# Performance work log

Hardware: AMD Instinct MI355X
Metric: run time of the kernel (lower is better)

## Reference

```python
import jax, jax.numpy as jnp
import numpy as np

IN_DIM, HID, OUT_DIM, NUM_LAYERS = 768, 512, 768, 4
B, T = 128, 256
EPS = 1e-5


def setup_inputs() -> dict:
    key = jax.random.key(0)
    ks = jax.random.split(key, 16)
    s = 0.02
    inp = {
        "x": jax.random.normal(ks[0], (B, T, IN_DIM), dtype=jnp.float32),
        "h0": jnp.zeros((NUM_LAYERS, B, HID), dtype=jnp.float32),
        "c0": jnp.zeros((NUM_LAYERS, B, HID), dtype=jnp.float32),
        "W_in": jax.random.normal(ks[1], (HID, IN_DIM), dtype=jnp.float32) * s,
        "b_in": jnp.zeros((HID,), dtype=jnp.float32),
        # stacked LSTM weights: all layers take HID input (after input_proj)
        "W_ih": jax.random.normal(ks[2], (NUM_LAYERS, 4 * HID, HID), dtype=jnp.float32) * s,
        "W_hh": jax.random.normal(ks[3], (NUM_LAYERS, 4 * HID, HID), dtype=jnp.float32) * s,
        "b_ih": jnp.zeros((NUM_LAYERS, 4 * HID), dtype=jnp.float32),
        "b_hh": jnp.zeros((NUM_LAYERS, 4 * HID), dtype=jnp.float32),
        "W_out": jax.random.normal(ks[4], (OUT_DIM, HID), dtype=jnp.float32) * s,
        "b_out": jnp.zeros((OUT_DIM,), dtype=jnp.float32),
        "ln_g": jnp.ones((OUT_DIM,), dtype=jnp.float32),
        "ln_b": jnp.zeros((OUT_DIM,), dtype=jnp.float32),
    }
    return inp


def _lstm_layer(x_seq, h0, c0, Wih, Whh, bih, bhh):
    # x_seq: [B,T,H] -> outputs [B,T,H], (hT, cT)
    bias = bih + bhh  # fuse the two biases

    def step(carry, x_t):
        h, c = carry
        gates = x_t @ Wih.T + h @ Whh.T + bias  # [B,4H]
        i, f, g, o = jnp.split(gates, 4, axis=-1)  # PyTorch gate order i,f,g,o
        i = jax.nn.sigmoid(i)
        f = jax.nn.sigmoid(f)
        g = jnp.tanh(g)
        o = jax.nn.sigmoid(o)
        c = f * c + i * g
        h = o * jnp.tanh(c)
        return (h, c), h

    (hT, cT), hs = jax.lax.scan(step, (h0, c0), jnp.swapaxes(x_seq, 0, 1))
    return jnp.swapaxes(hs, 0, 1), hT, cT


def reference(x, h0, c0, W_in, b_in, W_ih, W_hh, b_ih, b_hh, W_out, b_out, ln_g, ln_b):
    # input projection
    h = x @ W_in.T + b_in  # [B,T,HID]
    h_finals, c_finals = [], []
    for l in range(NUM_LAYERS):  # fixed small layer count; dropout inactive (eval)
        h, hT, cT = _lstm_layer(h, h0[l], c0[l], W_ih[l], W_hh[l], b_ih[l], b_hh[l])
        h_finals.append(hT)
        c_finals.append(cT)
    out = h @ W_out.T + b_out  # [B,T,OUT]
    mu = jnp.mean(out, axis=-1, keepdims=True)
    var = jnp.mean(jnp.square(out - mu), axis=-1, keepdims=True)
    out = (out - mu) * jax.lax.rsqrt(var + EPS) * ln_g + ln_b
    return out, jnp.stack(h_finals), jnp.stack(c_finals)
```

## Files before the change

### kernel.cpp

```cpp
#include <hip/hip_runtime.h>
#include <math.h>

#define T_SEQ 256
#define BATCH 128
#define HID 512
#define NL 4
#define HT_OFF 25165824u
#define CT_OFF 25427968u
#define HALL_ELEMS 67371008u
#define XP_ELEMS   16777216u
#define FLG_OFF(l,t) ((((l) << 8) + (t)) << 6)

typedef __attribute__((ext_vector_type(8))) short bf16x8;
typedef __attribute__((ext_vector_type(4))) float f32x4;

__device__ __forceinline__ short f2bf(float f) {
    unsigned u = __float_as_uint(f);
    u = (u + 0x7fffu + ((u >> 16) & 1u)) >> 16;
    return (short)u;
}
__device__ __forceinline__ unsigned pack2(float a, float b) {
    return ((unsigned)(unsigned short)f2bf(a)) |
           (((unsigned)(unsigned short)f2bf(b)) << 16);
}
__device__ __forceinline__ bf16x8 ld8_sc1g(const short* p) {
    unsigned long long q0 = __hip_atomic_load((const unsigned long long*)p,
                                              __ATOMIC_RELAXED, __HIP_MEMORY_SCOPE_AGENT);
    unsigned long long q1 = __hip_atomic_load((const unsigned long long*)(p + 512),
                                              __ATOMIC_RELAXED, __HIP_MEMORY_SCOPE_AGENT);
    union { unsigned long long q[2]; bf16x8 v; } u;
    u.q[0] = q0; u.q[1] = q1;
    return u.v;
}
__device__ __forceinline__ void poll_cnt4(const unsigned* base, int lane) {
    const unsigned* p = base + ((lane & 3) << 4);
    unsigned v = __hip_atomic_load(p, __ATOMIC_RELAXED, __HIP_MEMORY_SCOPE_AGENT);
    while (__any(v < 16u)) {
        __builtin_amdgcn_s_sleep(1);
        v = __hip_atomic_load(p, __ATOMIC_RELAXED, __HIP_MEMORY_SCOPE_AGENT);
    }
    asm volatile("" ::: "memory");
}
__device__ __forceinline__ void lds_wait(int* p, int want) {
    while (__hip_atomic_load(p, __ATOMIC_ACQUIRE, __HIP_MEMORY_SCOPE_WORKGROUP) < want)
        __builtin_amdgcn_s_sleep(1);
    asm volatile("" ::: "memory");
}

__global__ void init_kernel(short* __restrict__ h_all, unsigned* __restrict__ flg,
                            const float* __restrict__ h0) {
    int idx = blockIdx.x * 256 + threadIdx.x;
    if (idx < NL * BATCH * HID) {
        int l = idx >> 16, rest = idx & 65535;
        int r = rest >> 9, k = rest & 511;
        h_all[((size_t)(l * 257) << 16) + (((size_t)(k >> 2)) << 9) + (r << 2) + (k & 3)]
            = f2bf(h0[idx]);
    }
    if (idx < NL * T_SEQ * 64) flg[idx] = 0u;
}

__global__ __launch_bounds__(256) void gemm_xp(const float* __restrict__ x,
                                               const float* __restrict__ W_in,
                                               const float* __restrict__ b_in,
                                               short* __restrict__ xp) {
    __shared__ short As[128 * 72];
    __shared__ short Bs[128 * 72];
    const int tid = threadIdx.x;
    const int w = tid >> 6, lane = tid & 63;
    const int m = lane & 15, quad = lane >> 4;
    const int rowbase = blockIdx.x * 128;
    const int colbase = blockIdx.y * 128;
    f32x4 acc[2][8];
#pragma unroll
    for (int rt = 0; rt < 2; ++rt)
#pragma unroll
        for (int ct = 0; ct < 8; ++ct) { f32x4 z = {0.f,0.f,0.f,0.f}; acc[rt][ct] = z; }

    for (int k0 = 0; k0 < 768; k0 += 64) {
        __syncthreads();
#pragma unroll
        for (int i = 0; i < 8; ++i) {
            int q = tid + (i << 8);
            int r = q >> 4, f4 = (q & 15) << 2;
            float4 v = *(const float4*)(x + (size_t)(rowbase + r) * 768 + k0 + f4);
            uint2 p; p.x = pack2(v.x, v.y); p.y = pack2(v.z, v.w);
            *(uint2*)&As[r * 72 + f4] = p;
        }
#pragma unroll
        for (int i = 0; i < 8; ++i) {
            int q = tid + (i << 8);
            int r = q >> 4, f4 = (q & 15) << 2;
            float4 v = *(const float4*)(W_in + (size_t)(colbase + r) * 768 + k0 + f4);
            uint2 p; p.x = pack2(v.x, v.y); p.y = pack2(v.z, v.w);
            *(uint2*)&Bs[r * 72 + f4] = p;
        }
        __syncthreads();
#pragma unroll
        for (int ks = 0; ks < 2; ++ks) {
            int kof = (ks << 5) + (quad << 3);
            bf16x8 a0 = *(const bf16x8*)&As[((w * 2 + 0) * 16 + m) * 72 + kof];
            bf16x8 a1 = *(const bf16x8*)&As[((w * 2 + 1) * 16 + m) * 72 + kof];
#pragma unroll
            for (int ct = 0; ct < 8; ++ct) {
                bf16x8 b = *(const bf16x8*)&Bs[(ct * 16 + m) * 72 + kof];
                acc[0][ct] = __builtin_amdgcn_mfma_f32_16x16x32_bf16(a0, b, acc[0][ct], 0, 0, 0);
                acc[1][ct] = __builtin_amdgcn_mfma_f32_16x16x32_bf16(a1, b, acc[1][ct], 0, 0, 0);
            }
        }
    }
    float bias_r[8];
#pragma unroll
    for (int ct = 0; ct < 8; ++ct) bias_r[ct] = b_in[colbase + ct * 16 + m];
#pragma unroll
    for (int rt = 0; rt < 2; ++rt)
#pragma unroll
        for (int reg = 0; reg < 4; ++reg) {
            int m_glob = rowbase + (w * 2 + rt) * 16 + quad * 4 + reg;
            int t = m_glob & 255, b = m_glob >> 8;
            short* dst = xp + (((size_t)(t << 7) + b) << 9);
#pragma unroll
            for (int ct = 0; ct < 8; ++ct)
                dst[colbase + ct * 16 + m] = f2bf(acc[rt][ct][reg] + bias_r[ct]);
        }
}

__global__ __launch_bounds__(256) void gemm_out(const short* __restrict__ h3,
                                                const float* __restrict__ W_out,
                                                const float* __restrict__ b_out,
                                                float* __restrict__ out) {
    __shared__ short As[128 * 72];
    __shared__ short Bs[128 * 72];
    const int tid = threadIdx.x;
    const int w = tid >> 6, lane = tid & 63;
    const int m = lane & 15, quad = lane >> 4;
    const int rowbase = blockIdx.x * 128;
    const int colbase = blockIdx.y * 128;
    f32x4 acc[2][8];
#pragma unroll
    for (int rt = 0; rt < 2; ++rt)
#pragma unroll
        for (int ct = 0; ct < 8; ++ct) { f32x4 z = {0.f,0.f,0.f,0.f}; acc[rt][ct] = z; }

    for (int k0 = 0; k0 < 512; k0 += 64) {
        __syncthreads();
#pragma unroll
        for (int i = 0; i < 4; ++i) {
            int q = tid + (i << 8);
            int r = q >> 3, seg = (q & 7) << 3;
            *(bf16x8*)&As[r * 72 + seg] =
                *(const bf16x8*)(h3 + (size_t)(rowbase + r) * 512 + k0 + seg);
        }
#pragma unroll
        for (int i = 0; i < 8; ++i) {
            int q = tid + (i << 8);
            int r = q >> 4, f4 = (q & 15) << 2;
            float4 v = *(const float4*)(W_out + (size_t)(colbase + r) * 512 + k0 + f4);
            uint2 p; p.x = pack2(v.x, v.y); p.y = pack2(v.z, v.w);
            *(uint2*)&Bs[r * 72 + f4] = p;
        }
        __syncthreads();
#pragma unroll
        for (int ks = 0; ks < 2; ++ks) {
            int kof = (ks << 5) + (quad << 3);
            bf16x8 a0 = *(const bf16x8*)&As[((w * 2 + 0) * 16 + m) * 72 + kof];
            bf16x8 a1 = *(const bf16x8*)&As[((w * 2 + 1) * 16 + m) * 72 + kof];
#pragma unroll
            for (int ct = 0; ct < 8; ++ct) {
                bf16x8 b = *(const bf16x8*)&Bs[(ct * 16 + m) * 72 + kof];
                acc[0][ct] = __builtin_amdgcn_mfma_f32_16x16x32_bf16(a0, b, acc[0][ct], 0, 0, 0);
                acc[1][ct] = __builtin_amdgcn_mfma_f32_16x16x32_bf16(a1, b, acc[1][ct], 0, 0, 0);
            }
        }
    }
    float bias_r[8];
#pragma unroll
    for (int ct = 0; ct < 8; ++ct) bias_r[ct] = b_out[colbase + ct * 16 + m];
#pragma unroll
    for (int rt = 0; rt < 2; ++rt)
#pragma unroll
        for (int reg = 0; reg < 4; ++reg) {
            int m_glob = rowbase + (w * 2 + rt) * 16 + quad * 4 + reg;
            int t = m_glob >> 7, b = m_glob & 127;
            float* dst = out + (size_t)b * 196608 + (size_t)t * 768;
#pragma unroll
            for (int ct = 0; ct < 8; ++ct)
                dst[colbase + ct * 16 + m] = acc[rt][ct][reg] + bias_r[ct];
        }
}

__global__ __launch_bounds__(512, 2) void lstm_pipeline(
    short* __restrict__ xp, short* __restrict__ h_all,
    unsigned* __restrict__ flg,
    const float* __restrict__ W_ih, const float* __restrict__ W_hh,
    const float* __restrict__ b_ih, const float* __restrict__ b_hh,
    const float* __restrict__ c0, float* __restrict__ d_out) {
    __shared__ float gatesX[128 * 33];
    __shared__ float gatesH[128 * 33];
    __shared__ float cL[128 * 8];
    __shared__ float biasL[32];
    __shared__ int ldsdep[2];

    const int tid = threadIdx.x;
    const int l = blockIdx.x >> 6, c = blockIdx.x & 63;
    const int w = tid >> 6, lane = tid & 63;
    const int m = lane & 15, quad = lane >> 4;
    const bool hw = (w >= 4);
    const int w2 = w & 3;

    const float* Wsrc = hw ? W_hh : W_ih;
    bf16x8 wf[32];
#pragma unroll
    for (int ks = 0; ks < 16; ++ks) {
#pragma unroll
        for (int ct = 0; ct < 2; ++ct) {
            int u = ct * 16 + m;
            int gr = ((u >> 3) << 9) + (c << 3) + (u & 7);
            const float* s = Wsrc + ((size_t)(l * 2048 + gr) << 9) + ks * 32 + quad * 8;
            float4 v0 = *(const float4*)s;
            float4 v1 = *(const float4*)(s + 4);
            uint4 p;
            p.x = pack2(v0.x, v0.y); p.y = pack2(v0.z, v0.w);
            p.z = pack2(v1.x, v1.y); p.w = pack2(v1.z, v1.w);
            wf[ks * 2 + ct] = *(bf16x8*)&p;
        }
    }
    if (tid < 32) {
        int gr = ((tid >> 3) << 9) + (c << 3) + (tid & 7);
        biasL[tid] = b_ih[l * 2048 + gr] + b_hh[l * 2048 + gr];
    }
    if (tid < 2) ldsdep[tid] = 0;
    for (int p = tid; p < 1024; p += 512) {
        int r = p >> 3, hc = p & 7;
        cL[p] = c0[((size_t)l << 16) + (r << 9) + (c << 3) + hc];
    }
    __syncthreads();

    const int er = tid >> 2, eq = (tid & 3) << 1;

    for (int t = 0; t < T_SEQ; ++t) {
        if (hw) {
            if (t > 0) {
                if (w == 4) {
                    poll_cnt4(flg + FLG_OFF(l, t - 1), lane);
                    __hip_atomic_store(&ldsdep[1], t, __ATOMIC_RELEASE,
                                       __HIP_MEMORY_SCOPE_WORKGROUP);
                } else {
                    lds_wait(&ldsdep[1], t);
                }
            }
        } else if (l > 0) {
            if (w == 0) {
                poll_cnt4(flg + FLG_OFF(l - 1, t), lane);
                __hip_atomic_store(&ldsdep[0], t + 1, __ATOMIC_RELEASE,
                                   __HIP_MEMORY_SCOPE_WORKGROUP);
            } else {
                lds_wait(&ldsdep[0], t + 1);
            }
        }
        asm volatile("" ::: "memory");

        f32x4 z = {0.f, 0.f, 0.f, 0.f};
        f32x4 acc00 = z, acc01 = z, acc10 = z, acc11 = z;

        if (!hw && l == 0) {
            const short* src = xp + ((size_t)t << 16);
#pragma unroll
            for (int ks = 0; ks < 16; ++ks) {
                int ka = ks * 32 + quad * 8;
                bf16x8 a0 = *(const bf16x8*)(src + ((size_t)(w2 * 32 + m) << 9) + ka);
                bf16x8 a1 = *(const bf16x8*)(src + ((size_t)(w2 * 32 + 16 + m) << 9) + ka);
                acc00 = __builtin_amdgcn_mfma_f32_16x16x32_bf16(a0, wf[ks * 2 + 0], acc00, 0, 0, 0);
                acc01 = __builtin_amdgcn_mfma_f32_16x16x32_bf16(a0, wf[ks * 2 + 1], acc01, 0, 0, 0);
                acc10 = __builtin_amdgcn_mfma_f32_16x16x32_bf16(a1, wf[ks * 2 + 0], acc10, 0, 0, 0);
                acc11 = __builtin_amdgcn_mfma_f32_16x16x32_bf16(a1, wf[ks * 2 + 1], acc11, 0, 0, 0);
            }
        } else {
            const short* src = hw
                ? (h_all + ((size_t)(l * 257 + t) << 16))
                : (h_all + ((size_t)((l - 1) * 257 + t + 1) << 16));
#pragma unroll
            for (int ks = 0; ks < 16; ++ks) {
                int g = ks * 8 + quad * 2;
                const short* p = src + ((size_t)g << 9) + ((w2 * 32 + m) << 2);
                bf16x8 a0 = ld8_sc1g(p);
                bf16x8 a1 = ld8_sc1g(p + 64);
                acc00 = __builtin_amdgcn_mfma_f32_16x16x32_bf16(a0, wf[ks * 2 + 0], acc00, 0, 0, 0);
                acc01 = __builtin_amdgcn_mfma_f32_16x16x32_bf16(a0, wf[ks * 2 + 1], acc01, 0, 0, 0);
                acc10 = __builtin_amdgcn_mfma_f32_16x16x32_bf16(a1, wf[ks * 2 + 0], acc10, 0, 0, 0);
                acc11 = __builtin_amdgcn_mfma_f32_16x16x32_bf16(a1, wf[ks * 2 + 1], acc11, 0, 0, 0);
            }
        }
        const int gb0 = w2 * 32 + quad * 4;
        float* gdst = hw ? gatesH : gatesX;
#pragma unroll
        for (int reg = 0; reg < 4; ++reg) {
            gdst[(gb0 + reg) * 33 + m]           = acc00[reg];
            gdst[(gb0 + reg) * 33 + 16 + m]      = acc01[reg];
            gdst[(gb0 + 16 + reg) * 33 + m]      = acc10[reg];
            gdst[(gb0 + 16 + reg) * 33 + 16 + m] = acc11[reg];
        }
        __syncthreads();

        float hv[2], cv[2];
#pragma unroll
        for (int e = 0; e < 2; ++e) {
            int hc = eq + e;
            float iv = gatesX[er * 33 + hc]      + gatesH[er * 33 + hc]      + biasL[hc];
            float fv = gatesX[er * 33 + 8 + hc]  + gatesH[er * 33 + 8 + hc]  + biasL[8 + hc];
            float gv = gatesX[er * 33 + 16 + hc] + gatesH[er * 33 + 16 + hc] + biasL[16 + hc];
            float ov = gatesX[er * 33 + 24 + hc] + gatesH[er * 33 + 24 + hc] + biasL[24 + hc];
            float ig = 1.f / (1.f + __expf(-iv));
            float fg = 1.f / (1.f + __expf(-fv));
            float gg = tanhf(gv);
            float og = 1.f / (1.f + __expf(-ov));
            float cn = fg * cL[er * 8 + hc] + ig * gg;
            float hn = og * tanhf(cn);
            cL[er * 8 + hc] = cn;
            hv[e] = hn; cv[e] = cn;
        }
        unsigned pk = pack2(hv[0], hv[1]);
        {
            int g = c * 2 + (eq >> 2);
            unsigned* hdst = (unsigned*)(h_all + ((size_t)(l * 257 + t + 1) << 16)
                                         + ((size_t)g << 9) + (er << 2) + (eq & 3));
            __hip_atomic_store(hdst, pk, __ATOMIC_RELAXED, __HIP_MEMORY_SCOPE_AGENT);
        }
        if (l == 3) {
            unsigned* xdst = (unsigned*)(xp + ((size_t)t << 16) + (er << 9) + (c << 3) + eq);
            __hip_atomic_store(xdst, pk, __ATOMIC_RELAXED, __HIP_MEMORY_SCOPE_AGENT);
        }
        if (t == T_SEQ - 1) {
            size_t fo = ((size_t)l << 16) + (size_t)(er << 9) + (c << 3) + eq;
            d_out[HT_OFF + fo]     = hv[0];
            d_out[HT_OFF + fo + 1] = hv[1];
            d_out[CT_OFF + fo]     = cv[0];
            d_out[CT_OFF + fo + 1] = cv[1];
        }
        __syncthreads();
        if (tid == 0)
            __hip_atomic_fetch_add(flg + FLG_OFF(l, t) + ((c >> 4) << 4), 1u,
                                   __ATOMIC_RELAXED, __HIP_MEMORY_SCOPE_AGENT);
    }
}

__global__ __launch_bounds__(256) void ln_kernel(float* __restrict__ out,
                                                 const float* __restrict__ g,
                                                 const float* __restrict__ bvec) {
    float* p = out + (size_t)blockIdx.x * 768;
    int tid = threadIdx.x;
    float v0 = p[tid], v1 = p[tid + 256], v2 = p[tid + 512];
    float s = v0 + v1 + v2;
    float q = v0 * v0 + v1 * v1 + v2 * v2;
    for (int off = 32; off > 0; off >>= 1) {
        s += __shfl_down(s, off);
        q += __shfl_down(q, off);
    }
    __shared__ float ss[4], qq[4];
    __shared__ float mu_s, rs_s;
    int w = tid >> 6;
    if ((tid & 63) == 0) { ss[w] = s; qq[w] = q; }
    __syncthreads();
    if (tid == 0) {
        float S = ss[0] + ss[1] + ss[2] + ss[3];
        float Q = qq[0] + qq[1] + qq[2] + qq[3];
        float mu = S * (1.f / 768.f);
        float var = Q * (1.f / 768.f) - mu * mu;
        mu_s = mu;
        rs_s = rsqrtf(var + 1e-5f);
    }
    __syncthreads();
    float mu = mu_s, rs = rs_s;
    p[tid]       = (v0 - mu) * rs * g[tid]       + bvec[tid];
    p[tid + 256] = (v1 - mu) * rs * g[tid + 256] + bvec[tid + 256];
    p[tid + 512] = (v2 - mu) * rs * g[tid + 512] + bvec[tid + 512];
}

extern "C" void kernel_launch(void* const* d_in, const int* in_sizes, int n_in,
                              void* d_out, int out_size, void* d_ws, size_t ws_size,
                              hipStream_t stream) {
    (void)in_sizes; (void)n_in; (void)out_size; (void)ws_size;
    const float* x     = (const float*)d_in[0];
    const float* h0    = (const float*)d_in[1];
    const float* c0    = (const float*)d_in[2];
    const float* W_in  = (const float*)d_in[3];
    const float* b_in  = (const float*)d_in[4];
    const float* W_ih  = (const float*)d_in[5];
    const float* W_hh  = (const float*)d_in[6];
    const float* b_ih  = (const float*)d_in[7];
    const float* b_hh  = (const float*)d_in[8];
    const float* W_out = (const float*)d_in[9];
    const float* b_out = (const float*)d_in[10];
    const float* ln_g  = (const float*)d_in[11];
    const float* ln_b  = (const float*)d_in[12];

    float* out   = (float*)d_out;
    short* h_all = (short*)d_ws;
    short* xp    = h_all + HALL_ELEMS;
    unsigned* flg = (unsigned*)(xp + XP_ELEMS);

    init_kernel<<<1024, 256, 0, stream>>>(h_all, flg, h0);
    gemm_xp<<<dim3(256, 4), 256, 0, stream>>>(x, W_in, b_in, xp);
    lstm_pipeline<<<256, 512, 0, stream>>>(xp, h_all, flg, W_ih, W_hh,
                                           b_ih, b_hh, c0, out);
    gemm_out<<<dim3(256, 6), 256, 0, stream>>>(xp, W_out, b_out, out);
    ln_kernel<<<32768, 256, 0, stream>>>(out, ln_g, ln_b);
}
```

Before: 3.030 ms.

## Software-pipeline h loads, pad LDS strides, use fast tanh, relax launch bounds

Splits the recurrent matvec's global h loads into four chunks that are double-buffered, so loads of later chunks are issued while MFMAs run on earlier ones. LDS gate and cell buffers get padded strides (35 and 9) to reduce bank conflicts. tanhf is replaced by an exp-based fast tanh, which adds a small approximation error. Launch bounds drop from two blocks per CU to one, giving the compiler more registers for the extra prefetch buffers.

```diff
diff --git a/kernel.cpp b/kernel.cpp
--- a/kernel.cpp
+++ b/kernel.cpp
@@ -14,6 +14,8 @@
 typedef __attribute__((ext_vector_type(8))) short bf16x8;
 typedef __attribute__((ext_vector_type(4))) float f32x4;
 
+#define GSTR 35
+
 __device__ __forceinline__ short f2bf(float f) {
     unsigned u = __float_as_uint(f);
     u = (u + 0x7fffu + ((u >> 16) & 1u)) >> 16;
@@ -45,6 +47,10 @@
     while (__hip_atomic_load(p, __ATOMIC_ACQUIRE, __HIP_MEMORY_SCOPE_WORKGROUP) < want)
         __builtin_amdgcn_s_sleep(1);
     asm volatile("" ::: "memory");
+}
+__device__ __forceinline__ float tanh_fast(float x) {
+    float t = __expf(-2.f * fabsf(x));
+    return copysignf((1.f - t) / (1.f + t), x);
 }
 
 __global__ void init_kernel(short* __restrict__ h_all, unsigned* __restrict__ flg,
@@ -188,15 +194,34 @@
         }
 }
 
-__global__ __launch_bounds__(512, 2) void lstm_pipeline(
+#define LOADQ(A0_, A1_, kb_)                                                  \
+    _Pragma("unroll")                                                         \
+    for (int kk = 0; kk < 4; ++kk) {                                          \
+        int ks = (kb_) * 4 + kk;                                              \
+        int g = ks * 8 + quad * 2;                                            \
+        const short* pq = src + ((size_t)g << 9) + ((w2 * 32 + m) << 2);      \
+        A0_[kk] = ld8_sc1g(pq);                                               \
+        A1_[kk] = ld8_sc1g(pq + 64);                                          \
+    }
+#define COMPQ(A0_, A1_, kb_)                                                  \
+    _Pragma("unroll")                                                         \
+    for (int kk = 0; kk < 4; ++kk) {                                          \
+        int ks = (kb_) * 4 + kk;                                              \
+        acc00 = __builtin_amdgcn_mfma_f32_16x16x32_bf16(A0_[kk], wf[ks*2+0], acc00, 0, 0, 0); \
+        acc01 = __builtin_amdgcn_mfma_f32_16x16x32_bf16(A0_[kk], wf[ks*2+1], acc01, 0, 0, 0); \
+        acc10 = __builtin_amdgcn_mfma_f32_16x16x32_bf16(A1_[kk], wf[ks*2+0], acc10, 0, 0, 0); \
+        acc11 = __builtin_amdgcn_mfma_f32_16x16x32_bf16(A1_[kk], wf[ks*2+1], acc11, 0, 0, 0); \
+    }
+
+__global__ __launch_bounds__(512, 1) void lstm_pipeline(
     short* __restrict__ xp, short* __restrict__ h_all,
     unsigned* __restrict__ flg,
     const float* __restrict__ W_ih, const float* __restrict__ W_hh,
     const float* __restrict__ b_ih, const float* __restrict__ b_hh,
     const float* __restrict__ c0, float* __restrict__ d_out) {
-    __shared__ float gatesX[128 * 33];
-    __shared__ float gatesH[128 * 33];
-    __shared__ float cL[128 * 8];
+    __shared__ float gatesX[128 * GSTR];
+    __shared__ float gatesH[128 * GSTR];
+    __shared__ float cL[128 * 9];
     __shared__ float biasL[32];
     __shared__ int ldsdep[2];
 
@@ -231,7 +256,7 @@
     if (tid < 2) ldsdep[tid] = 0;
     for (int p = tid; p < 1024; p += 512) {
         int r = p >> 3, hc = p & 7;
-        cL[p] = c0[((size_t)l << 16) + (r << 9) + (c << 3) + hc];
+        cL[r * 9 + hc] = c0[((size_t)l << 16) + (r << 9) + (c << 3) + hc];
     }
     __syncthreads();
 
@@ -278,26 +303,24 @@
             const short* src = hw
                 ? (h_all + ((size_t)(l * 257 + t) << 16))
                 : (h_all + ((size_t)((l - 1) * 257 + t + 1) << 16));
-#pragma unroll
-            for (int ks = 0; ks < 16; ++ks) {
-                int g = ks * 8 + quad * 2;
-                const short* p = src + ((size_t)g << 9) + ((w2 * 32 + m) << 2);
-                bf16x8 a0 = ld8_sc1g(p);
-                bf16x8 a1 = ld8_sc1g(p + 64);
-                acc00 = __builtin_amdgcn_mfma_f32_16x16x32_bf16(a0, wf[ks * 2 + 0], acc00, 0, 0, 0);
-                acc01 = __builtin_amdgcn_mfma_f32_16x16x32_bf16(a0, wf[ks * 2 + 1], acc01, 0, 0, 0);
-                acc10 = __builtin_amdgcn_mfma_f32_16x16x32_bf16(a1, wf[ks * 2 + 0], acc10, 0, 0, 0);
-                acc11 = __builtin_amdgcn_mfma_f32_16x16x32_bf16(a1, wf[ks * 2 + 1], acc11, 0, 0, 0);
-            }
+            bf16x8 Pa[4], Pb[4], Qa[4], Qb[4];
+            LOADQ(Pa, Pb, 0)
+            LOADQ(Qa, Qb, 1)
+            COMPQ(Pa, Pb, 0)
+            LOADQ(Pa, Pb, 2)
+            COMPQ(Qa, Qb, 1)
+            LOADQ(Qa, Qb, 3)
+            COMPQ(Pa, Pb, 2)
+            COMPQ(Qa, Qb, 3)
         }
         const int gb0 = w2 * 32 + quad * 4;
         float* gdst = hw ? gatesH : gatesX;
 #pragma unroll
         for (int reg = 0; reg < 4; ++reg) {
-            gdst[(gb0 + reg) * 33 + m]           = acc00[reg];
-            gdst[(gb0 + reg) * 33 + 16 + m]      = acc01[reg];
-            gdst[(gb0 + 16 + reg) * 33 + m]      = acc10[reg];
-            gdst[(gb0 + 16 + reg) * 33 + 16 + m] = acc11[reg];
+            gdst[(gb0 + reg) * GSTR + m]           = acc00[reg];
+            gdst[(gb0 + reg) * GSTR + 16 + m]      = acc01[reg];
+            gdst[(gb0 + 16 + reg) * GSTR + m]      = acc10[reg];
+            gdst[(gb0 + 16 + reg) * GSTR + 16 + m] = acc11[reg];
         }
         __syncthreads();
 
@@ -305,17 +328,17 @@
 #pragma unroll
         for (int e = 0; e < 2; ++e) {
             int hc = eq + e;
-            float iv = gatesX[er * 33 + hc]      + gatesH[er * 33 + hc]      + biasL[hc];
-            float fv = gatesX[er * 33 + 8 + hc]  + gatesH[er * 33 + 8 + hc]  + biasL[8 + hc];
-            float gv = gatesX[er * 33 + 16 + hc] + gatesH[er * 33 + 16 + hc] + biasL[16 + hc];
-            float ov = gatesX[er * 33 + 24 + hc] + gatesH[er * 33 + 24 + hc] + biasL[24 + hc];
+            float iv = gatesX[er * GSTR + hc]      + gatesH[er * GSTR + hc]      + biasL[hc];
+            float fv = gatesX[er * GSTR + 8 + hc]  + gatesH[er * GSTR + 8 + hc]  + biasL[8 + hc];
+            float gv = gatesX[er * GSTR + 16 + hc] + gatesH[er * GSTR + 16 + hc] + biasL[16 + hc];
+            float ov = gatesX[er * GSTR + 24 + hc] + gatesH[er * GSTR + 24 + hc] + biasL[24 + hc];
             float ig = 1.f / (1.f + __expf(-iv));
             float fg = 1.f / (1.f + __expf(-fv));
-            float gg = tanhf(gv);
+            float gg = tanh_fast(gv);
             float og = 1.f / (1.f + __expf(-ov));
-            float cn = fg * cL[er * 8 + hc] + ig * gg;
-            float hn = og * tanhf(cn);
-            cL[er * 8 + hc] = cn;
+            float cn = fg * cL[er * 9 + hc] + ig * gg;
+            float hn = og * tanh_fast(cn);
+            cL[er * 9 + hc] = cn;
             hv[e] = hn; cv[e] = cn;
         }
         unsigned pk = pack2(hv[0], hv[1]);
```

Result: faster. 2.894 ms (-4.5%).
